# Performance work log

Hardware: AMD Instinct MI355X
Metric: run time of the kernel (lower is better)

## Reference

```python
import jax, jax.numpy as jnp
import numpy as np

NUM_HEADS = 16

def setup_inputs() -> dict:
    key = jax.random.key(0)
    k_x, k_wq, k_bq, k_wo, k_bo = jax.random.split(key, 5)
    B, S, D = 4, 2048, 1024
    x = jax.random.normal(k_x, (B, S, D), dtype=jnp.float32)
    # Flax Dense default init: lecun_normal for kernel, zeros for bias; use small normals here.
    w_qkv = jax.random.normal(k_wq, (D, 3 * D), dtype=jnp.float32) * (D ** -0.5)
    b_qkv = jnp.zeros((3 * D,), dtype=jnp.float32)
    w_out = jax.random.normal(k_wo, (D, D), dtype=jnp.float32) * (D ** -0.5)
    b_out = jnp.zeros((D,), dtype=jnp.float32)
    return {"x": x, "w_qkv": w_qkv, "b_qkv": b_qkv, "w_out": w_out, "b_out": b_out}

def reference(x, w_qkv, b_qkv, w_out, b_out):
    B, S, D = x.shape
    H = NUM_HEADS
    hd = D // H
    scale = hd ** -0.5
    qkv = x @ w_qkv + b_qkv                                  # [B,S,3D]
    qkv = qkv.reshape(B, S, 3, H, hd)
    qkv = jnp.transpose(qkv, (2, 0, 3, 1, 4))                # [3,B,H,S,hd]
    q, k, v = qkv[0], qkv[1], qkv[2]
    attn = jnp.einsum("bhqd,bhkd->bhqk", q, k) * scale       # [B,H,S,S]
    attn = jax.nn.softmax(attn, axis=-1)
    out = jnp.einsum("bhqk,bhkd->bhqd", attn, v)             # [B,H,S,hd]
    out = jnp.transpose(out, (0, 2, 1, 3)).reshape(B, S, D)
    return out @ w_out + b_out
```

## Files before the change

kernel.cpp:

```cpp
#include <hip/hip_runtime.h>
#include <cstdint>
#include <cstddef>

#define B_    4
#define S_    2048
#define D_    1024
#define H_    16
#define HD_   64
#define M_    8192
#define NQKV  3072

typedef __bf16 bf16;
typedef __bf16 bf16x4 __attribute__((ext_vector_type(4)));
typedef __bf16 bf16x8 __attribute__((ext_vector_type(8)));
typedef float  f32x4  __attribute__((ext_vector_type(4)));
typedef float  f32x16 __attribute__((ext_vector_type(16)));
typedef unsigned short u16x4 __attribute__((ext_vector_type(4)));
typedef uint32_t u32x4 __attribute__((ext_vector_type(4)));

__device__ __forceinline__ void gl2lds16(const void* g, void* l) {
  __builtin_amdgcn_global_load_lds(
      (__attribute__((address_space(1))) void*)(uintptr_t)g,
      (__attribute__((address_space(3))) void*)l, 16, 0, 0);
}

__device__ __forceinline__ uint32_t pkbf16(float a, float b) {
  union { bf16 h[2]; uint32_t u; } z;
  z.h[0] = (bf16)a; z.h[1] = (bf16)b;
  return z.u;
}

__global__ __launch_bounds__(256) void cast_f32_bf16(const float* __restrict__ in,
                                                     bf16* __restrict__ out, int n4) {
  int i = blockIdx.x * 256 + threadIdx.x;
  if (i >= n4) return;
  float4 v = ((const float4*)in)[i];
  bf16x4 o;
  o[0] = (bf16)v.x; o[1] = (bf16)v.y; o[2] = (bf16)v.z; o[3] = (bf16)v.w;
  ((bf16x4*)out)[i] = o;
}

__global__ __launch_bounds__(256) void transpose_cast(const float* __restrict__ in,
                                                      bf16* __restrict__ out, int R, int C) {
  __shared__ float tile[32][33];
  int bx = blockIdx.x * 32, by = blockIdx.y * 32;
  int tx = threadIdx.x, ty = threadIdx.y;
#pragma unroll
  for (int i = 0; i < 32; i += 8)
    tile[ty + i][tx] = in[(size_t)(by + ty + i) * C + bx + tx];
  __syncthreads();
#pragma unroll
  for (int i = 0; i < 32; i += 8)
    out[(size_t)(bx + ty + i) * R + by + tx] = (bf16)tile[tx][ty + i];
}

template <bool OUT_BF16>
__global__ __launch_bounds__(256) void gemm_bt(const bf16* __restrict__ A,
                                               const bf16* __restrict__ Bt,
                                               const float* __restrict__ bias,
                                               void* __restrict__ Cptr,
                                               int M, int N, int K) {
  __shared__ __align__(16) bf16 As[128 * 64];
  __shared__ __align__(16) bf16 Bs[128 * 64];
  const int tid  = threadIdx.x;
  const int lane = tid & 63, w = tid >> 6;
  const int lo   = lane & 15, quad = lane >> 4;
  const int xcd = blockIdx.x & 7, g = blockIdx.x >> 3;
  const int mi  = g & 7,          n = g >> 3;
  const int bm  = (xcd * 8 + mi) * 128, bn = n * 128;
  const int wm = (w >> 1) * 64,    wn = (w & 1) * 64;

  f32x4 acc[4][4];
  const f32x4 zero = {0.f, 0.f, 0.f, 0.f};
#pragma unroll
  for (int i = 0; i < 4; ++i)
#pragma unroll
    for (int j = 0; j < 4; ++j) acc[i][j] = zero;

  for (int k0 = 0; k0 < K; k0 += 64) {
#pragma unroll
    for (int c = 0; c < 4; ++c) {
      int seg = c * 4 + w;
      int idx = seg * 512 + lane * 8;
      int row = idx >> 6, col = idx & 63;
      gl2lds16(A  + (size_t)(bm + row) * K + k0 + col, As + seg * 512);
      gl2lds16(Bt + (size_t)(bn + row) * K + k0 + col, Bs + seg * 512);
    }
    __syncthreads();
#pragma unroll
    for (int ks = 0; ks < 2; ++ks) {
      bf16x8 av[4], bv[4];
#pragma unroll
      for (int i = 0; i < 4; ++i)
        av[i] = *(const bf16x8*)&As[(wm + i * 16 + lo) * 64 + ks * 32 + quad * 8];
#pragma unroll
      for (int j = 0; j < 4; ++j)
        bv[j] = *(const bf16x8*)&Bs[(wn + j * 16 + lo) * 64 + ks * 32 + quad * 8];
#pragma unroll
      for (int i = 0; i < 4; ++i)
#pragma unroll
        for (int j = 0; j < 4; ++j)
          acc[i][j] = __builtin_amdgcn_mfma_f32_16x16x32_bf16(av[i], bv[j], acc[i][j], 0, 0, 0);
    }
    __syncthreads();
  }
#pragma unroll
  for (int j = 0; j < 4; ++j) {
    int cg = bn + wn + j * 16 + lo;
    float bsv = bias[cg];
#pragma unroll
    for (int i = 0; i < 4; ++i) {
      int rg = bm + wm + i * 16 + quad * 4;
#pragma unroll
      for (int r = 0; r < 4; ++r) {
        float v = acc[i][j][r] + bsv;
        if (OUT_BF16) ((bf16*)Cptr)[(size_t)(rg + r) * N + cg] = (bf16)v;
        else          ((float*)Cptr)[(size_t)(rg + r) * N + cg] = v;
      }
    }
  }
}

#define PSTR 72

__global__ __launch_bounds__(256, 4) void flash_attn(const bf16* __restrict__ qkv,
                                                     bf16* __restrict__ out) {
  __shared__ __align__(16) bf16 Ks[2][64 * 64];
  __shared__ __align__(16) bf16 Vs[2][64 * PSTR];

  const int tid  = threadIdx.x;
  const int lane = tid & 63, wq = tid >> 6;
  const int l31  = lane & 31;
  const int e    = lane >> 5;
  const int hi8  = e * 8, hi4 = e * 4;

  const int bid = blockIdx.x;
  const int qb  = bid >> 6;
  const int bh  = bid & 63;
  const int h   = bh & 15;
  const int b   = bh >> 4;
  const int q0  = qb * 128;
  const size_t rowb = (size_t)b * S_;
  const bf16* qbase = qkv + rowb * NQKV + h * HD_;
  const bf16* kbase = qbase + D_;
  const bf16* vbase = qbase + 2 * D_;

  bf16x8 qf[4];
  {
    const bf16* qrow = qbase + (size_t)(q0 + wq * 32 + l31) * NQKV;
#pragma unroll
    for (int c = 0; c < 4; ++c)
      qf[c] = *(const bf16x8*)(qrow + c * 16 + hi8);
  }

  int kq_off[2];
#pragma unroll
  for (int it = 0; it < 2; ++it) {
    int ci = it * 256 + tid;
    int s  = ci >> 3;
    int x  = (ci & 7) ^ (s & 7);
    kq_off[it] = s * NQKV + x * 8;
  }
  int vs_d[2], vs_s[2];
#pragma unroll
  for (int u = 0; u < 2; ++u) {
    int idx = u * 256 + tid;
    vs_d[u] = (idx & 31) * 2;
    vs_s[u] = (idx >> 5) * 4;
  }

  uint32_t vreg[2][4];

#pragma unroll
  for (int it = 0; it < 2; ++it)
    gl2lds16(kbase + kq_off[it], &Ks[0][(it * 256 + wq * 64) * 8]);
#pragma unroll
  for (int u = 0; u < 2; ++u)
#pragma unroll
    for (int j = 0; j < 4; ++j)
      vreg[u][j] = *(const uint32_t*)(vbase + (size_t)(vs_s[u] + j) * NQKV + vs_d[u]);

  const f32x16 zero16 = {0.f,0.f,0.f,0.f,0.f,0.f,0.f,0.f,0.f,0.f,0.f,0.f,0.f,0.f,0.f,0.f};
  f32x16 oacc[2];
  oacc[0] = zero16; oacc[1] = zero16;
  float lsum = 0.f;
  const float c2 = 0.125f * 1.44269504088896341f;

  for (int kt = 0; kt < 32; ++kt) {
    const int buf = kt & 1;
#pragma unroll
    for (int u = 0; u < 2; ++u) {
      int d0 = vs_d[u], s0 = vs_s[u];
      u16x4 lo, hi;
#pragma unroll
      for (int j = 0; j < 4; ++j) {
        lo[j] = (unsigned short)(vreg[u][j] & 0xffffu);
        hi[j] = (unsigned short)(vreg[u][j] >> 16);
      }
      *(u16x4*)&Vs[buf][(d0 + 0) * PSTR + s0] = lo;
      *(u16x4*)&Vs[buf][(d0 + 1) * PSTR + s0] = hi;
    }
    __syncthreads();

    {
      int ktn = (kt + 1 < 32) ? kt + 1 : 31;
      const bf16* kb = kbase + (size_t)ktn * 64 * NQKV;
#pragma unroll
      for (int it = 0; it < 2; ++it)
        gl2lds16(kb + kq_off[it], &Ks[buf ^ 1][(it * 256 + wq * 64) * 8]);
    }
    {
      int ktn = (kt + 1 < 32) ? kt + 1 : 31;
      const bf16* vb = vbase + (size_t)ktn * 64 * NQKV;
#pragma unroll
      for (int u = 0; u < 2; ++u)
#pragma unroll
        for (int j = 0; j < 4; ++j)
          vreg[u][j] = *(const uint32_t*)(vb + (size_t)(vs_s[u] + j) * NQKV + vs_d[u]);
    }

    f32x16 sacc[2];
#pragma unroll
    for (int kk = 0; kk < 2; ++kk) {
      sacc[kk] = zero16;
      int srow = kk * 32 + l31;
      int swz  = (srow & 7) * 8;
#pragma unroll
      for (int c = 0; c < 4; ++c) {
        bf16x8 kf = *(const bf16x8*)&Ks[buf][srow * 64 + ((c * 16 + hi8) ^ swz)];
        sacc[kk] = __builtin_amdgcn_mfma_f32_32x32x16_bf16(kf, qf[c], sacc[kk], 0, 0, 0);
      }
    }

#pragma unroll
    for (int kk = 0; kk < 2; ++kk) {
      uint32_t Q8[8];
      float ps = 0.f;
#pragma unroll
      for (int i = 0; i < 8; ++i) {
        float p0 = __builtin_amdgcn_exp2f(sacc[kk][2 * i]     * c2 - 16.0f);
        float p1 = __builtin_amdgcn_exp2f(sacc[kk][2 * i + 1] * c2 - 16.0f);
        ps += p0 + p1;
        Q8[i] = pkbf16(p0, p1);
      }
      lsum += ps;
#pragma unroll
      for (int mh = 0; mh < 2; ++mh) {
        const int m = kk * 2 + mh, bq = mh * 4;
        uint32_t s0 = e ? Q8[bq]     : Q8[bq + 2];
        uint32_t s1 = e ? Q8[bq + 1] : Q8[bq + 3];
        uint32_t r0 = __shfl_xor(s0, 32);
        uint32_t r1 = __shfl_xor(s1, 32);
        u32x4 pd;
        pd[0] = e ? r0 : Q8[bq];
        pd[1] = e ? r1 : Q8[bq + 1];
        pd[2] = e ? Q8[bq + 2] : r0;
        pd[3] = e ? Q8[bq + 3] : r1;
        bf16x8 pf = __builtin_bit_cast(bf16x8, pd);
#pragma unroll
        for (int dt = 0; dt < 2; ++dt) {
          int drow = dt * 32 + l31;
          bf16x8 vf = *(const bf16x8*)&Vs[buf][drow * PSTR + m * 16 + hi8];
          oacc[dt] = __builtin_amdgcn_mfma_f32_32x32x16_bf16(vf, pf, oacc[dt], 0, 0, 0);
        }
      }
    }
  }

  lsum += __shfl_xor(lsum, 32);

  __syncthreads();
  bf16* Os = (bf16*)Vs;
  {
    float inv = 1.f / lsum;
    int ql = wq * 32 + l31;
#pragma unroll
    for (int dt = 0; dt < 2; ++dt) {
#pragma unroll
      for (int g = 0; g < 4; ++g) {
        bf16x4 ov;
#pragma unroll
        for (int jj = 0; jj < 4; ++jj) ov[jj] = (bf16)(oacc[dt][g * 4 + jj] * inv);
        *(bf16x4*)&Os[ql * PSTR + dt * 32 + g * 8 + hi4] = ov;
      }
    }
  }
  __syncthreads();
#pragma unroll
  for (int it = 0; it < 4; ++it) {
    int idx = it * 256 + tid;
    int row = idx >> 3, c8 = (idx & 7) * 8;
    bf16x8 t = *(const bf16x8*)&Os[row * PSTR + c8];
    *(bf16x8*)&out[(rowb + q0 + row) * D_ + h * HD_ + c8] = t;
  }
}

extern "C" void kernel_launch(void* const* d_in, const int* in_sizes, int n_in,
                              void* d_out, int out_size, void* d_ws, size_t ws_size,
                              hipStream_t stream) {
  const float* x     = (const float*)d_in[0];
  const float* w_qkv = (const float*)d_in[1];
  const float* b_qkv = (const float*)d_in[2];
  const float* w_out = (const float*)d_in[3];
  const float* b_out = (const float*)d_in[4];
  float* out = (float*)d_out;

  char* ws = (char*)d_ws;
  bf16* xb    = (bf16*)(ws);
  bf16* wqkvT = (bf16*)(ws + (size_t)16777216);
  bf16* woutT = (bf16*)(ws + (size_t)23068672);
  bf16* qkvb  = (bf16*)(ws + (size_t)25165824);
  bf16* attnb = (bf16*)(ws + (size_t)75497472);

  cast_f32_bf16<<<(M_ * D_ / 4 + 255) / 256, 256, 0, stream>>>(x, xb, M_ * D_ / 4);
  transpose_cast<<<dim3(NQKV / 32, D_ / 32), dim3(32, 8), 0, stream>>>(w_qkv, wqkvT, D_, NQKV);
  transpose_cast<<<dim3(D_ / 32, D_ / 32), dim3(32, 8), 0, stream>>>(w_out, woutT, D_, D_);

  gemm_bt<true><<<(M_ / 128) * (NQKV / 128), 256, 0, stream>>>(
      xb, wqkvT, b_qkv, (void*)qkvb, M_, NQKV, D_);

  flash_attn<<<B_ * H_ * (S_ / 128), 256, 0, stream>>>(qkvb, attnb);

  gemm_bt<false><<<(M_ / 128) * (D_ / 128), 256, 0, stream>>>(
      attnb, woutT, b_out, (void*)out, M_, D_, D_);
}
```

Baseline: 306.3 us.

## Add wide 128x256 QKV GEMM tile and XOR-swizzle attention V/O LDS layout

Adds a new QKV projection GEMM kernel that uses 128x256 output tiles per block with an XCD-aware block mapping, so each staged A tile is reused across more columns. It raises register pressure and drops occupancy to 2 blocks per CU. Separately, the flash attention V and output LDS buffers switch from a padded stride of 72 to an unpadded 64-wide layout with an XOR swizzle, which shrinks shared memory and is meant to avoid bank conflicts. The new GEMM keeps a single LDS buffer with no prefetch double-buffering, so load latency may not be hidden.

After: 303.3 us. About the same (-1.0%).

```diff
diff --git a/kernel.cpp b/kernel.cpp
--- a/kernel.cpp
+++ b/kernel.cpp
@@ -121,12 +121,79 @@
   }
 }
 
-#define PSTR 72
+__global__ __launch_bounds__(256, 2) void gemm_bt_wide(const bf16* __restrict__ A,
+                                                       const bf16* __restrict__ Bt,
+                                                       const float* __restrict__ bias,
+                                                       bf16* __restrict__ Cptr,
+                                                       int M, int N, int K) {
+  __shared__ __align__(16) bf16 As[128 * 64];
+  __shared__ __align__(16) bf16 Bs[256 * 64];
+  const int tid  = threadIdx.x;
+  const int lane = tid & 63, w = tid >> 6;
+  const int lo   = lane & 15, quad = lane >> 4;
+  const int xcd = blockIdx.x & 7, g = blockIdx.x >> 3;
+  const int mi  = g & 7,          n = g >> 3;
+  const int bm  = (xcd * 8 + mi) * 128, bn = n * 256;
+  const int wm = (w >> 1) * 64,    wn = (w & 1) * 128;
+
+  f32x4 acc[4][8];
+  const f32x4 zero = {0.f, 0.f, 0.f, 0.f};
+#pragma unroll
+  for (int i = 0; i < 4; ++i)
+#pragma unroll
+    for (int j = 0; j < 8; ++j) acc[i][j] = zero;
+
+  for (int k0 = 0; k0 < K; k0 += 64) {
+#pragma unroll
+    for (int c = 0; c < 4; ++c) {
+      int seg = c * 4 + w;
+      int idx = seg * 512 + lane * 8;
+      int row = idx >> 6, col = idx & 63;
+      gl2lds16(A + (size_t)(bm + row) * K + k0 + col, As + seg * 512);
+    }
+#pragma unroll
+    for (int c = 0; c < 8; ++c) {
+      int seg = c * 4 + w;
+      int idx = seg * 512 + lane * 8;
+      int row = idx >> 6, col = idx & 63;
+      gl2lds16(Bt + (size_t)(bn + row) * K + k0 + col, Bs + seg * 512);
+    }
+    __syncthreads();
+#pragma unroll
+    for (int ks = 0; ks < 2; ++ks) {
+      bf16x8 av[4], bv[8];
+#pragma unroll
+      for (int i = 0; i < 4; ++i)
+        av[i] = *(const bf16x8*)&As[(wm + i * 16 + lo) * 64 + ks * 32 + quad * 8];
+#pragma unroll
+      for (int j = 0; j < 8; ++j)
+        bv[j] = *(const bf16x8*)&Bs[(wn + j * 16 + lo) * 64 + ks * 32 + quad * 8];
+#pragma unroll
+      for (int i = 0; i < 4; ++i)
+#pragma unroll
+        for (int j = 0; j < 8; ++j)
+          acc[i][j] = __builtin_amdgcn_mfma_f32_16x16x32_bf16(av[i], bv[j], acc[i][j], 0, 0, 0);
+    }
+    __syncthreads();
+  }
+#pragma unroll
+  for (int j = 0; j < 8; ++j) {
+    int cg = bn + wn + j * 16 + lo;
+    float bsv = bias[cg];
+#pragma unroll
+    for (int i = 0; i < 4; ++i) {
+      int rg = bm + wm + i * 16 + quad * 4;
+#pragma unroll
+      for (int r = 0; r < 4; ++r)
+        Cptr[(size_t)(rg + r) * N + cg] = (bf16)(acc[i][j][r] + bsv);
+    }
+  }
+}
 
 __global__ __launch_bounds__(256, 4) void flash_attn(const bf16* __restrict__ qkv,
                                                      bf16* __restrict__ out) {
   __shared__ __align__(16) bf16 Ks[2][64 * 64];
-  __shared__ __align__(16) bf16 Vs[2][64 * PSTR];
+  __shared__ __align__(16) bf16 Vs[2][64 * 64];
 
   const int tid  = threadIdx.x;
   const int lane = tid & 63, wq = tid >> 6;
@@ -161,12 +228,15 @@
     int x  = (ci & 7) ^ (s & 7);
     kq_off[it] = s * NQKV + x * 8;
   }
-  int vs_d[2], vs_s[2];
+  int vs_d[2], vs_s[2], vs_off[2];
 #pragma unroll
   for (int u = 0; u < 2; ++u) {
     int idx = u * 256 + tid;
-    vs_d[u] = (idx & 31) * 2;
-    vs_s[u] = (idx >> 5) * 4;
+    int d0 = (idx & 31) * 2;
+    int s0 = (idx >> 5) * 4;
+    vs_d[u] = d0;
+    vs_s[u] = s0;
+    vs_off[u] = (((s0 >> 3) ^ ((d0 >> 1) & 7)) * 8) + (s0 & 7);
   }
 
   uint32_t vreg[2][4];
@@ -190,15 +260,15 @@
     const int buf = kt & 1;
 #pragma unroll
     for (int u = 0; u < 2; ++u) {
-      int d0 = vs_d[u], s0 = vs_s[u];
+      int d0 = vs_d[u];
       u16x4 lo, hi;
 #pragma unroll
       for (int j = 0; j < 4; ++j) {
         lo[j] = (unsigned short)(vreg[u][j] & 0xffffu);
         hi[j] = (unsigned short)(vreg[u][j] >> 16);
       }
-      *(u16x4*)&Vs[buf][(d0 + 0) * PSTR + s0] = lo;
-      *(u16x4*)&Vs[buf][(d0 + 1) * PSTR + s0] = hi;
+      *(u16x4*)&Vs[buf][(d0 + 0) * 64 + vs_off[u]] = lo;
+      *(u16x4*)&Vs[buf][(d0 + 1) * 64 + vs_off[u]] = hi;
     }
     __syncthreads();
 
@@ -260,7 +330,8 @@
 #pragma unroll
         for (int dt = 0; dt < 2; ++dt) {
           int drow = dt * 32 + l31;
-          bf16x8 vf = *(const bf16x8*)&Vs[buf][drow * PSTR + m * 16 + hi8];
+          int swv  = (drow >> 1) & 7;
+          bf16x8 vf = *(const bf16x8*)&Vs[buf][drow * 64 + (((m * 2 + e) ^ swv) * 8)];
           oacc[dt] = __builtin_amdgcn_mfma_f32_32x32x16_bf16(vf, pf, oacc[dt], 0, 0, 0);
         }
       }
@@ -274,6 +345,7 @@
   {
     float inv = 1.f / lsum;
     int ql = wq * 32 + l31;
+    int swO = (ql >> 1) & 7;
 #pragma unroll
     for (int dt = 0; dt < 2; ++dt) {
 #pragma unroll
@@ -281,7 +353,7 @@
         bf16x4 ov;
 #pragma unroll
         for (int jj = 0; jj < 4; ++jj) ov[jj] = (bf16)(oacc[dt][g * 4 + jj] * inv);
-        *(bf16x4*)&Os[ql * PSTR + dt * 32 + g * 8 + hi4] = ov;
+        *(bf16x4*)&Os[ql * 64 + (((dt * 4 + g) ^ swO) * 8) + hi4] = ov;
       }
     }
   }
@@ -289,9 +361,9 @@
 #pragma unroll
   for (int it = 0; it < 4; ++it) {
     int idx = it * 256 + tid;
-    int row = idx >> 3, c8 = (idx & 7) * 8;
-    bf16x8 t = *(const bf16x8*)&Os[row * PSTR + c8];
-    *(bf16x8*)&out[(rowb + q0 + row) * D_ + h * HD_ + c8] = t;
+    int row = idx >> 3, c8 = idx & 7;
+    bf16x8 t = *(const bf16x8*)&Os[row * 64 + ((c8 ^ ((row >> 1) & 7)) * 8)];
+    *(bf16x8*)&out[(rowb + q0 + row) * D_ + h * HD_ + c8 * 8] = t;
   }
 }
 
@@ -316,8 +388,8 @@
   transpose_cast<<<dim3(NQKV / 32, D_ / 32), dim3(32, 8), 0, stream>>>(w_qkv, wqkvT, D_, NQKV);
   transpose_cast<<<dim3(D_ / 32, D_ / 32), dim3(32, 8), 0, stream>>>(w_out, woutT, D_, D_);
 
-  gemm_bt<true><<<(M_ / 128) * (NQKV / 128), 256, 0, stream>>>(
-      xb, wqkvT, b_qkv, (void*)qkvb, M_, NQKV, D_);
+  gemm_bt_wide<<<(M_ / 128) * (NQKV / 256), 256, 0, stream>>>(
+      xb, wqkvT, b_qkv, qkvb, M_, NQKV, D_);
 
   flash_attn<<<B_ * H_ * (S_ / 128), 256, 0, stream>>>(qkvb, attnb);
 
```
